# Kernel tuning notes

Measured on AMD Instinct MI355X. Metric: run time of the kernel, lower is better.

Reference implementation:

```python
import jax, jax.numpy as jnp
import numpy as np

B, S, D_MODEL, N_HEADS = 4, 2048, 512, 2
D4 = D_MODEL * 4            # output dim of quaternion projections (2048)
HD = D4 // N_HEADS          # per-head dim (1024)
EPS = 1e-6


def quat_linear(x, W, b):
    """Hamilton-product quaternion linear.
    x: [..., 4*in_q] (quaternions interleaved r,i,j,k)
    W: [4, out_q, in_q] components (r,i,j,k); b: [4*out_q]
    returns [..., 4*out_q]
    """
    xq = x.reshape(x.shape[:-1] + (-1, 4))
    xr, xi, xj, xk = xq[..., 0], xq[..., 1], xq[..., 2], xq[..., 3]
    Wr, Wi, Wj, Wk = W[0], W[1], W[2], W[3]
    m = lambda a, M: jnp.einsum('...i,oi->...o', a, M)
    o_r = m(xr, Wr) - m(xi, Wi) - m(xj, Wj) - m(xk, Wk)
    o_i = m(xr, Wi) + m(xi, Wr) + m(xj, Wk) - m(xk, Wj)
    o_j = m(xr, Wj) - m(xi, Wk) + m(xj, Wr) + m(xk, Wi)
    o_k = m(xr, Wk) + m(xi, Wj) - m(xj, Wi) + m(xk, Wr)
    out = jnp.stack([o_r, o_i, o_j, o_k], axis=-1)
    return out.reshape(out.shape[:-2] + (-1,)) + b


def setup_inputs() -> dict:
    rng = jax.random.key(0)
    ks = jax.random.split(rng, 12)
    def w(k, out_q, in_q):
        return jax.random.normal(k, (4, out_q, in_q), jnp.float32) * (1.0 / np.sqrt(4.0 * in_q))
    in_q_small = D_MODEL // 4   # q/k/v projections: d_model reals -> d_model quaternions
    in_q_big = D4 // 4          # later projections: 4*d_model reals -> d_model quaternions
    zb = jnp.zeros((D4,), jnp.float32)
    return {
        'query': jax.random.normal(ks[0], (B, S, D_MODEL), jnp.float32),
        'key':   jax.random.normal(ks[1], (B, S, D_MODEL), jnp.float32),
        'value': jax.random.normal(ks[2], (B, S, D_MODEL), jnp.float32),
        'Wq': w(ks[3], D_MODEL, in_q_small), 'bq': zb,
        'Wk': w(ks[4], D_MODEL, in_q_small), 'bk': zb,
        'Wv': w(ks[5], D_MODEL, in_q_small), 'bv': zb,
        'alpha': jax.random.normal(ks[6], (D4,), jnp.float32) * 0.1,
        'Wint': w(ks[7], D_MODEL, in_q_big), 'bint': zb,
        'Wfin': w(ks[8], D_MODEL, in_q_big), 'bfin': zb,
        'Wout': w(ks[9], D_MODEL, in_q_big), 'bout': zb,
    }


def reference(query, key, value, Wq, bq, Wk, bk, Wv, bv, alpha,
              Wint, bint, Wfin, bfin, Wout, bout):
    Q = quat_linear(query, Wq, bq).reshape(B, S, N_HEADS, HD)
    K = quat_linear(key, Wk, bk).reshape(B, S, N_HEADS, HD)
    V = quat_linear(value, Wv, bv).reshape(B, S, N_HEADS, HD)

    # spectral attention: FFT correlation + adaptive spectral filter
    Qf = jnp.fft.fft(Q, axis=1)
    Kf = jnp.fft.fft(K, axis=1)
    corr = Qf * jnp.conj(Kf)                        # [B,S,H,HD] complex64
    freqs = jnp.abs(jnp.fft.fftfreq(S))             # [S]
    phase = jnp.arctan(jnp.log(freqs + EPS))        # [S]
    a = alpha.reshape(N_HEADS, HD)
    filt = jnp.exp(1j * (phase[:, None, None] * a[None, :, :]))  # [S,H,HD]
    attn_w = jnp.fft.ifft(corr * filt[None], axis=1).real        # [B,S,H,HD]
    attn = (attn_w * V).reshape(B, S, -1)           # [B,S,4*d_model]

    attn = quat_linear(attn, Wint, bint)
    attn = quat_linear(attn, Wfin, bfin)
    return quat_linear(attn, Wout, bout)            # [B,S,4*d_model]
```

## Files before the change

kernel.cpp:

```cpp
#include <hip/hip_runtime.h>
#include <hip/hip_bf16.h>
#include <cstdint>

typedef unsigned short u16;
typedef u16  u16x4 __attribute__((ext_vector_type(4)));
typedef u16  u16x8 __attribute__((ext_vector_type(8)));
typedef short s16x8 __attribute__((ext_vector_type(8)));
typedef float f32x4 __attribute__((ext_vector_type(4)));

#define PI_F 3.14159265358979323846f
#define PD(i) ((i) + 3 * ((i) >> 5))

static __device__ __forceinline__ u16 f2bf(float f) {
    union { float f; unsigned u; } v; v.f = f;
    unsigned r = v.u + 0x7fffu + ((v.u >> 16) & 1u);
    return (u16)(r >> 16);
}
static __device__ __forceinline__ float bf2f(u16 h) {
    union { unsigned u; float f; } v; v.u = ((unsigned)h) << 16;
    return v.f;
}

__device__ __forceinline__ void gl_lds16(const u16* g, u16* l) {
    __builtin_amdgcn_global_load_lds(
        (const __attribute__((address_space(1))) unsigned int*)g,
        (__attribute__((address_space(3))) unsigned int*)l, 16, 0, 0);
}

__device__ __forceinline__ void cvt_body(int blk, const float* __restrict__ in,
                                         u16* __restrict__ o) {
    int i = blk * 256 + threadIdx.x;
    float4 a = ((const float4*)in)[2 * i];
    float4 b = ((const float4*)in)[2 * i + 1];
    u16x8 vv;
    vv[0] = f2bf(a.x); vv[1] = f2bf(a.y); vv[2] = f2bf(a.z); vv[3] = f2bf(a.w);
    vv[4] = f2bf(b.x); vv[5] = f2bf(b.y); vv[6] = f2bf(b.z); vv[7] = f2bf(b.w);
    ((u16x8*)o)[i] = vv;
}

__device__ __forceinline__ void hamilton(int c, int cp, int& qmv, float& qsv) {
    const int   qm[4][4] = {{0,1,2,3},{1,0,3,2},{2,3,0,1},{3,2,1,0}};
    const float qs[4][4] = {{1.f,-1.f,-1.f,-1.f},{1.f,1.f,1.f,-1.f},
                            {1.f,-1.f,1.f,1.f},{1.f,1.f,-1.f,1.f}};
    qmv = qm[c][cp]; qsv = qs[c][cp];
}

template<int LOGK>
__device__ __forceinline__ void e3_body(int blk, const float* __restrict__ W,
                                        u16* __restrict__ E) {
    const int K = 1 << LOGK;
    int idx = blk * 256 + threadIdx.x;
    int n = idx >> LOGK, k = idx & (K - 1);
    int o = n >> 2, c = n & 3, i = k >> 2, cp = k & 3;
    int qmv; float qsv; hamilton(c, cp, qmv, qsv);
    int in_q = K >> 2;
    float w = W[(size_t)qmv * 512 * in_q + (size_t)o * in_q + i] * qsv;
    E[idx] = f2bf(w);
}

__device__ __forceinline__ void ytr_body(int blk, const float* __restrict__ W,
                                         u16* __restrict__ YT) {
    int b = blk * 256 + threadIdx.x;
    int row = b >> 9, o = b & 511;
    int cb = row >> 9, i = row & 511;
    YT[b] = f2bf(W[((size_t)cb * 512 + o) * 512 + i]);
}

__device__ __forceinline__ void tabs_body(int blk, float2* __restrict__ gws,
                                          float* __restrict__ ph) {
    int i = blk * 256 + threadIdx.x;
    if (i < 292) {
        int off, denom;
        if (i < 4)       { off = 0;  denom = 16;   }
        else if (i < 36) { off = 4;  denom = 128;  }
        else             { off = 36; denom = 1024; }
        float a = (-PI_F) * (float)(i - off) / (float)denom;
        gws[i] = make_float2(cosf(a), sinf(a));
    }
    if (i <= 1024) {
        ph[i] = atanf(logf((float)i * (1.0f / 2048.0f) + 1e-6f));
    }
}

__global__ __launch_bounds__(256) void fat_prep(
        const float* __restrict__ query, const float* __restrict__ key,
        const float* __restrict__ value, u16* __restrict__ Acvt,
        const float* __restrict__ Wq, const float* __restrict__ Wk,
        const float* __restrict__ Wv, u16* __restrict__ Eq,
        u16* __restrict__ Ek, u16* __restrict__ Ev,
        const float* __restrict__ Wint, const float* __restrict__ Wfin,
        const float* __restrict__ Wout, u16* __restrict__ Xfin,
        u16* __restrict__ Xout, u16* __restrict__ YtInt,
        float2* __restrict__ gws, float* __restrict__ pht) {
    int b = blockIdx.x;
    if (b < 6144) {
        int ten = b >> 11, r = b & 2047;
        const float* in = (ten == 0) ? query : (ten == 1) ? key : value;
        cvt_body(r, in, Acvt + (size_t)ten * 8192 * 512);
    } else if (b < 18432) {
        int rb = b - 6144;
        int y = rb >> 12, r = rb & 4095;
        e3_body<9>(r, (y == 0) ? Wq : (y == 1) ? Wk : Wv,
                   (y == 0) ? Eq : (y == 1) ? Ek : Ev);
    } else if (b < 18944) {
        cvt_body(b - 18432, Wfin, Xfin);
    } else if (b < 19456) {
        cvt_body(b - 18944, Wout, Xout);
    } else if (b < 23552) {
        ytr_body(b - 19456, Wint, YtInt);
    } else {
        tabs_body(b - 23552, gws, pht);
    }
}

__device__ __forceinline__ void mvW_body(int blk, const float* __restrict__ v,
                                         const float* __restrict__ W,
                                         const float* __restrict__ badd,
                                         float* __restrict__ out) {
    int n    = (blk * 256 + threadIdx.x) >> 6;
    int lane = threadIdx.x & 63;
    if (n >= 2048) return;
    int o = n >> 2, c = n & 3;
    int cp = lane & 3;
    int qmv; float qsv; hamilton(c, cp, qmv, qsv);
    const float* Wrow = W + ((size_t)qmv * 512 + o) * 512;
    float s = 0.f;
    for (int k = lane; k < 2048; k += 64) s += v[k] * Wrow[k >> 2];
    s *= qsv;
#pragma unroll
    for (int off = 32; off; off >>= 1) s += __shfl_down(s, off, 64);
    if (lane == 0) out[n] = s + badd[n];
}

template<int K, int OUTMODE, int NBY>
__device__ __forceinline__ void gemm_body(int bid, u16* As, u16* Bs,
                                          const u16* __restrict__ A,
                                          const u16* __restrict__ E,
                                          const float* __restrict__ bias,
                                          void* __restrict__ outp) {
    const int t    = threadIdx.x;
    const int lane = t & 63, wave = t >> 6;
    const int wr   = wave >> 1, wc = wave & 1;
    const int lr   = lane & 15, kg = lane >> 4;
    const int l7   = lr & 7;

    constexpr int SPX = (4 * (NBY / 4)) / 8;
    const int xcd = bid & 7, p = bid >> 3;
    const int st  = xcd * SPX + (p >> 4);
    const int w   = p & 15;
    const int bx  = (st & 3) * 4 + (w & 3);
    const int by  = (st >> 2) * 4 + (w >> 2);
    const int m0  = by * 128;
    const int n0  = bx * 128;

    f32x4 acc[4][4];
#pragma unroll
    for (int i = 0; i < 4; ++i)
#pragma unroll
        for (int j = 0; j < 4; ++j) acc[i][j] = (f32x4){0.f, 0.f, 0.f, 0.f};

    const int arow = wr * 64 + lr;
    const int brow = wc * 64 + lr;

    for (int k0 = 0; k0 < K; k0 += 64) {
#pragma unroll
        for (int c = 0; c < 4; ++c) {
            int idx = t + c * 256;
            int row = idx >> 3, sl = idx & 7;
            int gsl = sl ^ (row & 7);
            gl_lds16(A + (size_t)(m0 + row) * K + k0 + gsl * 8, &As[idx * 8]);
            gl_lds16(E + (size_t)(n0 + row) * K + k0 + gsl * 8, &Bs[idx * 8]);
        }
        __syncthreads();
#pragma unroll
        for (int ks = 0; ks < 2; ++ks) {
            const int slot = (ks * 4 + kg) ^ l7;
            s16x8 av[4], bv[4];
#pragma unroll
            for (int mi = 0; mi < 4; ++mi)
                av[mi] = *(const s16x8*)&As[(arow + mi * 16) * 64 + slot * 8];
#pragma unroll
            for (int ni = 0; ni < 4; ++ni)
                bv[ni] = *(const s16x8*)&Bs[(brow + ni * 16) * 64 + slot * 8];
#pragma unroll
            for (int mi = 0; mi < 4; ++mi)
#pragma unroll
                for (int ni = 0; ni < 4; ++ni)
                    acc[mi][ni] = __builtin_amdgcn_mfma_f32_16x16x32_bf16(
                        av[mi], bv[ni], acc[mi][ni], 0, 0, 0);
        }
        __syncthreads();
    }

#pragma unroll
    for (int ni = 0; ni < 4; ++ni) {
        int n = n0 + wc * 64 + ni * 16 + lr;
        float bvl = bias ? bias[n] : 0.0f;
#pragma unroll
        for (int mi = 0; mi < 4; ++mi) {
#pragma unroll
            for (int r = 0; r < 4; ++r) {
                int m = m0 + wr * 64 + mi * 16 + kg * 4 + r;
                float val = acc[mi][ni][r] + bvl;
                if constexpr (OUTMODE == 0) {
                    ((u16*)outp)[(size_t)m * 2048 + n] = f2bf(val);
                } else if constexpr (OUTMODE == 1) {
                    ((float*)outp)[(size_t)m * 2048 + n] = val;
                } else {
                    int b = m >> 11, s = m & 2047;
                    ((u16*)outp)[((size_t)b * 2048 + n) * 2048 + s] = f2bf(val);
                }
            }
        }
    }
}

template<int K, int OUTMODE, int NBY>
__global__ __launch_bounds__(256) void gemm2(const u16* __restrict__ A,
                                             const u16* __restrict__ E,
                                             const float* __restrict__ bias,
                                             void* __restrict__ outp) {
    __shared__ u16 As[128 * 64];
    __shared__ u16 Bs[128 * 64];
    gemm_body<K, OUTMODE, NBY>(blockIdx.x, As, Bs, A, E, bias, outp);
}

__global__ __launch_bounds__(256) void gemm_fatA(const u16* __restrict__ Aq,
                                                 const u16* __restrict__ Eq,
                                                 const float* __restrict__ bq,
                                                 void* __restrict__ Qt,
                                                 const u16* __restrict__ Ak,
                                                 const u16* __restrict__ Ek,
                                                 const float* __restrict__ bk,
                                                 void* __restrict__ Kt,
                                                 const u16* __restrict__ Xfin,
                                                 const u16* __restrict__ YtInt,
                                                 void* __restrict__ Z1,
                                                 const float* __restrict__ Wfin,
                                                 const float* __restrict__ bint,
                                                 const float* __restrict__ bfin,
                                                 float* __restrict__ bv1) {
    __shared__ u16 As[128 * 64];
    __shared__ u16 Bs[128 * 64];
    int bid = blockIdx.x;
    if (bid < 256) {
        gemm_body<512, 0, 16>(bid, As, Bs, Xfin, YtInt, nullptr, Z1);
    } else if (bid < 1280) {
        gemm_body<512, 2, 64>(bid - 256, As, Bs, Aq, Eq, bq, Qt);
    } else if (bid < 2304) {
        gemm_body<512, 2, 64>(bid - 1280, As, Bs, Ak, Ek, bk, Kt);
    } else {
        mvW_body(bid - 2304, bint, Wfin, bfin, bv1);
    }
}

__global__ __launch_bounds__(256) void qcomb1(const u16* __restrict__ Z1,
                                              u16* __restrict__ Yt2) {
    __shared__ float tile[32][33];
    const int CA[4][4] = {{0,1,2,3},{1,0,3,2},{2,0,1,3},{3,0,2,1}};
    const int CB[4][4] = {{0,1,2,3},{0,1,2,3},{0,2,3,1},{0,3,1,2}};
    const float SG[4][4] = {{1.f,-1.f,-1.f,-1.f},{1.f,1.f,1.f,-1.f},
                            {1.f,1.f,1.f,-1.f},{1.f,1.f,1.f,-1.f}};
    const int cm = blockIdx.z;
    const int p0 = blockIdx.x * 32, i0 = blockIdx.y * 32;
    const int tx = threadIdx.x, ty = threadIdx.y;
#pragma unroll
    for (int dy = 0; dy < 32; dy += 8) {
        int p = p0 + ty + dy;
        float acc = 0.f;
#pragma unroll
        for (int q = 0; q < 4; ++q)
            acc += SG[cm][q] * bf2f(Z1[(size_t)(CA[cm][q] * 512 + p) * 2048
                                       + CB[cm][q] * 512 + i0 + tx]);
        tile[ty + dy][tx] = acc;
    }
    __syncthreads();
#pragma unroll
    for (int dy = 0; dy < 32; dy += 8)
        Yt2[((size_t)cm * 512 + i0 + ty + dy) * 512 + p0 + tx]
            = f2bf(tile[tx][ty + dy]);
}

template<int LH, int OFF>
__device__ __forceinline__ void r8pass(float* re, float* im,
                                       const float2* __restrict__ wt, int t) {
    constexpr int h = 1 << LH;
    __syncthreads();
    const int j  = t & (h - 1);
    const int i0 = ((t >> LH) << (LH + 3)) | j;
    const float2 w = wt[OFF + j];
    const float t2r = w.x * w.x - w.y * w.y;
    const float t2i = 2.f * w.x * w.y;
    const float t1r = t2r * t2r - t2i * t2i;
    const float t1i = 2.f * t2r * t2i;
    const float S = 0.70710678118654752f;
    const float Ac = S * (w.x + w.y);
    const float Bc = S * (w.y - w.x);

    float xr[8], xi[8];
    int p[8];
#pragma unroll
    for (int k = 0; k < 8; ++k) {
        p[k] = PD(i0 + k * h);
        xr[k] = re[p[k]]; xi[k] = im[p[k]];
    }
#pragma unroll
    for (int kp = 0; kp < 8; kp += 2) {
        float tr = t1r * xr[kp + 1] - t1i * xi[kp + 1];
        float ti = t1r * xi[kp + 1] + t1i * xr[kp + 1];
        float ar = xr[kp], ai = xi[kp];
        xr[kp] = ar + tr;     xi[kp] = ai + ti;
        xr[kp + 1] = ar - tr; xi[kp + 1] = ai - ti;
    }
#pragma unroll
    for (int q = 0; q < 2; ++q) {
        int b0 = q * 4;
        {
            float tr = t2r * xr[b0 + 2] - t2i * xi[b0 + 2];
            float ti = t2r * xi[b0 + 2] + t2i * xr[b0 + 2];
            float ar = xr[b0], ai = xi[b0];
            xr[b0] = ar + tr;     xi[b0] = ai + ti;
            xr[b0 + 2] = ar - tr; xi[b0 + 2] = ai - ti;
        }
        {
            float tr = t2i * xr[b0 + 3] + t2r * xi[b0 + 3];
            float ti = t2i * xi[b0 + 3] - t2r * xr[b0 + 3];
            float ar = xr[b0 + 1], ai = xi[b0 + 1];
            xr[b0 + 1] = ar + tr; xi[b0 + 1] = ai + ti;
            xr[b0 + 3] = ar - tr; xi[b0 + 3] = ai - ti;
        }
    }
    {
        float tr = w.x * xr[4] - w.y * xi[4];
        float ti = w.x * xi[4] + w.y * xr[4];
        float ar = xr[0], ai = xi[0];
        xr[0] = ar + tr; xi[0] = ai + ti;
        xr[4] = ar - tr; xi[4] = ai - ti;
    }
    {
        float tr = Ac * xr[5] - Bc * xi[5];
        float ti = Ac * xi[5] + Bc * xr[5];
        float ar = xr[1], ai = xi[1];
        xr[1] = ar + tr; xi[1] = ai + ti;
        xr[5] = ar - tr; xi[5] = ai - ti;
    }
    {
        float tr = w.y * xr[6] + w.x * xi[6];
        float ti = w.y * xi[6] - w.x * xr[6];
        float ar = xr[2], ai = xi[2];
        xr[2] = ar + tr; xi[2] = ai + ti;
        xr[6] = ar - tr; xi[6] = ai - ti;
    }
    {
        float tr = Bc * xr[7] + Ac * xi[7];
        float ti = Bc * xi[7] - Ac * xr[7];
        float ar = xr[3], ai = xi[3];
        xr[3] = ar + tr; xi[3] = ai + ti;
        xr[7] = ar - tr; xi[7] = ai - ti;
    }
#pragma unroll
    for (int k = 0; k < 8; ++k) { re[p[k]] = xr[k]; im[p[k]] = xi[k]; }
}

__device__ void fft2048(float* re, float* im, const float2* __restrict__ wt, int t) {
    __syncthreads();
#pragma unroll
    for (int u = 0; u < 2; ++u) {
        int i0 = (t + u * 256) << 2;
        int p0 = PD(i0);
        float x0r = re[p0],     x0i = im[p0];
        float x1r = re[p0 + 1], x1i = im[p0 + 1];
        float x2r = re[p0 + 2], x2i = im[p0 + 2];
        float x3r = re[p0 + 3], x3i = im[p0 + 3];
        float ar = x0r + x1r, ai = x0i + x1i;
        float br = x0r - x1r, bi = x0i - x1i;
        float cr = x2r + x3r, ci = x2i + x3i;
        float dr = x2r - x3r, di = x2i - x3i;
        re[p0]     = ar + cr; im[p0]     = ai + ci;
        re[p0 + 2] = ar - cr; im[p0 + 2] = ai - ci;
        re[p0 + 1] = br + di; im[p0 + 1] = bi - dr;
        re[p0 + 3] = br - di; im[p0 + 3] = bi + dr;
    }
    r8pass<2, 0>(re, im, wt, t);
    r8pass<5, 4>(re, im, wt, t);
    r8pass<8, 36>(re, im, wt, t);
    __syncthreads();
}

__device__ void spectral_body(int sbid, float* zre, float* zim, float2* wt,
                              const u16* __restrict__ Qt,
                              const u16* __restrict__ Kt,
                              u16* __restrict__ Wt,
                              const float* __restrict__ alpha,
                              const float2* __restrict__ gws,
                              const float* __restrict__ gph) {
    const int t  = threadIdx.x;
    const int b  = sbid >> 10;
    const int cp = sbid & 1023;
    const int c0 = cp * 2;
    const size_t base0 = ((size_t)b * 2048 + c0) * 2048;
    const size_t base1 = base0 + 2048;

    for (int i = t; i < 292; i += 256) wt[i] = gws[i];

    float ph[4];
    float PH1r[4], PH1i[4], PH2r[4], PH2i[4];
    float ph24 = 0.f, PH24_1 = 0.f, PH24_2 = 0.f;

#pragma unroll
    for (int ch = 0; ch < 2; ++ch) {
        const size_t base = ch ? base1 : base0;
        const u16* Qp = Qt + base;
        const u16* Kp = Kt + base;
        __syncthreads();
#pragma unroll
        for (int u = 0; u < 8; ++u) {
            int s = t + u * 256;
            int r = __brev((unsigned)s) >> 21;
            zre[PD(r)] = bf2f(Qp[s]);
            zim[PD(r)] = bf2f(Kp[s]);
        }
        fft2048(zre, zim, wt, t);
        const float ac = alpha[c0 + ch];
#pragma unroll
        for (int u = 0; u < 4; ++u) {
            int k = t + u * 256;
            int m = (2048 - k) & 2047;
            float ar = zre[PD(k)], ai = zim[PD(k)];
            float br = zre[PD(m)], bi = zim[PD(m)];
            float qr = 0.5f * (ar + br), qi = 0.5f * (ai - bi);
            float kr = 0.5f * (ai + bi), ki = 0.5f * (br - ar);
            float cr = qr * kr + qi * ki;
            float ci = qi * kr - qr * ki;
            if (ch == 0) ph[u] = gph[min(k, 2048 - k)];
            float fr, fi;
            __sincosf(ph[u] * ac, &fi, &fr);
            float Pkr = cr * fr - ci * fi, Pki = cr * fi + ci * fr;
            float qr2 = 0.5f * (br + ar), qi2 = 0.5f * (bi - ai);
            float kr2 = 0.5f * (bi + ai), ki2 = 0.5f * (ar - br);
            float cr2 = qr2 * kr2 + qi2 * ki2;
            float ci2 = qi2 * kr2 - qr2 * ki2;
            float Pmr = cr2 * fr - ci2 * fi, Pmi = cr2 * fi + ci2 * fr;
            float hr = 0.5f * (Pkr + Pmr), hi = 0.5f * (Pki - Pmi);
            if (ch == 0) { PH1r[u] = hr; PH1i[u] = hi; }
            else         { PH2r[u] = hr; PH2i[u] = hi; }
        }
        if (t == 0) {
            float ar = zre[PD(1024)], ai = zim[PD(1024)];
            float cr = ar * ai;
            if (ch == 0) ph24 = gph[1024];
            float fr, fi;
            __sincosf(ph24 * ac, &fi, &fr);
            if (ch == 0) PH24_1 = cr * fr; else PH24_2 = cr * fr;
        }
    }

    __syncthreads();
#pragma unroll
    for (int u = 0; u < 4; ++u) {
        int k = t + u * 256;
        int m = (2048 - k) & 2047;
        int rk = __brev((unsigned)k) >> 21;
        int rm = __brev((unsigned)m) >> 21;
        zre[PD(rk)] = PH1r[u] - PH2i[u];
        zim[PD(rk)] = PH1i[u] + PH2r[u];
        zre[PD(rm)] = PH1r[u] + PH2i[u];
        zim[PD(rm)] = PH2r[u] - PH1i[u];
    }
    if (t == 0) {
        zre[PD(1)] = PH24_1;
        zim[PD(1)] = PH24_2;
    }
    fft2048(zre, zim, wt, t);

#pragma unroll
    for (int u = 0; u < 8; ++u) {
        int s = t + u * 256;
        int j = (2048 - s) & 2047;
        Wt[base0 + s] = f2bf(zre[PD(j)] * (1.0f / 2048.0f));
        Wt[base1 + s] = f2bf(zim[PD(j)] * (1.0f / 2048.0f));
    }
}

__global__ __launch_bounds__(256) void fat_specv(const u16* __restrict__ Qt,
                                                 const u16* __restrict__ Kt,
                                                 u16* __restrict__ Wt,
                                                 const float* __restrict__ alpha,
                                                 const float2* __restrict__ gws,
                                                 const float* __restrict__ gph,
                                                 const u16* __restrict__ Av,
                                                 const u16* __restrict__ Ev,
                                                 const float* __restrict__ bvb,
                                                 void* __restrict__ Vt,
                                                 const u16* __restrict__ Xout,
                                                 const u16* __restrict__ Yt2,
                                                 void* __restrict__ Z2,
                                                 const float* __restrict__ Wout,
                                                 const float* __restrict__ bv1,
                                                 const float* __restrict__ bout,
                                                 float* __restrict__ bv2) {
    __shared__ __align__(16) char smem[32768];
    int bid = blockIdx.x;
    if (bid < 256) {
        gemm_body<512, 0, 16>(bid, (u16*)smem, (u16*)(smem + 16384),
                              Xout, Yt2, nullptr, Z2);
        return;
    }
    if (bid >= 5376) {
        mvW_body(bid - 5376, bv1, Wout, bout, bv2);
        return;
    }
    bid -= 256;
    if (bid % 5 == 4) {
        gemm_body<512, 2, 64>(bid / 5, (u16*)smem, (u16*)(smem + 16384),
                              Av, Ev, bvb, Vt);
    } else {
        int sbid = (bid / 5) * 4 + (bid % 5);
        spectral_body(sbid, (float*)smem, (float*)(smem + 8960),
                      (float2*)(smem + 17920), Qt, Kt, Wt, alpha, gws, gph);
    }
}

__device__ __forceinline__ void qcomb2_body(int blk, const u16* __restrict__ Z2,
                                            u16* __restrict__ Ecomb) {
    int id = blk * 256 + threadIdx.x;
    int q = id >> 9, i = id & 511;
    float z[4][4];
#pragma unroll
    for (int ca = 0; ca < 4; ++ca)
#pragma unroll
        for (int cb = 0; cb < 4; ++cb)
            z[ca][cb] = bf2f(Z2[(size_t)(ca * 512 + q) * 2048 + cb * 512 + i]);
    float wc[4];
    wc[0] = z[0][0] - z[1][1] - z[2][2] - z[3][3];
    wc[1] = z[1][0] + z[0][1] + z[3][2] - z[2][3];
    wc[2] = z[2][0] + z[0][2] + z[1][3] - z[3][1];
    wc[3] = z[3][0] + z[0][3] + z[2][1] - z[1][2];
#pragma unroll
    for (int c = 0; c < 4; ++c) {
        u16x4 row;
#pragma unroll
        for (int cp = 0; cp < 4; ++cp) {
            int qmv; float qsv; hamilton(c, cp, qmv, qsv);
            row[cp] = f2bf(qsv * wc[qmv]);
        }
        *(u16x4*)&Ecomb[(size_t)(4 * q + c) * 2048 + 4 * i] = row;
    }
}

__device__ __forceinline__ void tmul_body(int blk, const u16* __restrict__ W,
                                          const u16* __restrict__ V,
                                          u16* __restrict__ out, u16* tile) {
    const int b  = blk >> 10;
    const int rem = blk & 1023;
    const int c0 = (rem & 31) * 64, s0 = (rem >> 5) * 64;
    const int t  = threadIdx.x;
    const int g  = (t & 15) * 4;
    const int rb = t >> 4;
#pragma unroll
    for (int r = 0; r < 4; ++r) {
        int c = rb + 16 * r;
        size_t idx = ((size_t)b * 2048 + c0 + c) * 2048 + s0 + g;
        u16x4 wv = *(const u16x4*)&W[idx];
        u16x4 vv = *(const u16x4*)&V[idx];
#pragma unroll
        for (int j = 0; j < 4; ++j)
            tile[c * 70 + g + j] = f2bf(bf2f(wv[j]) * bf2f(vv[j]));
    }
    __syncthreads();
#pragma unroll
    for (int r = 0; r < 4; ++r) {
        int s = rb + 16 * r;
        u16x4 o;
#pragma unroll
        for (int j = 0; j < 4; ++j) o[j] = tile[(g + j) * 70 + s];
        *(u16x4*)&out[((size_t)b * 2048 + s0 + s) * 2048 + c0 + g] = o;
    }
}

__global__ __launch_bounds__(256) void fat_post(const u16* __restrict__ Z2,
                                                u16* __restrict__ Ecomb,
                                                const u16* __restrict__ W,
                                                const u16* __restrict__ V,
                                                u16* __restrict__ attn) {
    __shared__ u16 tile[64 * 70];
    int bid = blockIdx.x;
    if (bid < 1024) qcomb2_body(bid, Z2, Ecomb);
    else            tmul_body(bid - 1024, W, V, attn, tile);
}

extern "C" void kernel_launch(void* const* d_in, const int* in_sizes, int n_in,
                              void* d_out, int out_size, void* d_ws, size_t ws_size,
                              hipStream_t stream) {
    const float* query = (const float*)d_in[0];
    const float* key   = (const float*)d_in[1];
    const float* value = (const float*)d_in[2];
    const float* Wq    = (const float*)d_in[3];
    const float* bq    = (const float*)d_in[4];
    const float* Wk    = (const float*)d_in[5];
    const float* bk    = (const float*)d_in[6];
    const float* Wv    = (const float*)d_in[7];
    const float* bv    = (const float*)d_in[8];
    const float* alpha = (const float*)d_in[9];
    const float* Wint  = (const float*)d_in[10];
    const float* bint  = (const float*)d_in[11];
    const float* Wfin  = (const float*)d_in[12];
    const float* bfin  = (const float*)d_in[13];
    const float* Wout  = (const float*)d_in[14];
    const float* bout  = (const float*)d_in[15];

    char* ws = (char*)d_ws;
    size_t off = 0;
    auto alloc = [&](size_t bytes) -> void* {
        void* p = ws + off;
        off += (bytes + 255) & ~(size_t)255;
        return p;
    };
    u16* Eq    = (u16*)alloc((size_t)2048 * 512 * 2);
    u16* Ek    = (u16*)alloc((size_t)2048 * 512 * 2);
    u16* Ev    = (u16*)alloc((size_t)2048 * 512 * 2);
    u16* Xfin  = (u16*)alloc((size_t)2048 * 512 * 2);
    u16* Xout  = (u16*)alloc((size_t)2048 * 512 * 2);
    u16* YtInt = (u16*)alloc((size_t)2048 * 512 * 2);
    u16* Yt2   = (u16*)alloc((size_t)2048 * 512 * 2);
    u16* Z1    = (u16*)alloc((size_t)2048 * 2048 * 2);
    u16* Z2    = (u16*)alloc((size_t)2048 * 2048 * 2);
    u16* Ecomb = (u16*)alloc((size_t)2048 * 2048 * 2);
    u16* Qt    = (u16*)alloc((size_t)4 * 2048 * 2048 * 2);
    u16* Kt    = (u16*)alloc((size_t)4 * 2048 * 2048 * 2);
    u16* Vt    = (u16*)alloc((size_t)4 * 2048 * 2048 * 2);
    u16* attn  = (u16*)alloc((size_t)8192 * 2048 * 2);
    float2* gws = (float2*)alloc(292 * 8);
    float*  pht = (float*)alloc(1025 * 4);
    float*  bv1 = (float*)alloc(2048 * 4);
    float*  bv2 = (float*)alloc(2048 * 4);
    u16* Wt = Qt;
    u16* Aq = attn;
    u16* Ak = attn + (size_t)8192 * 512;
    u16* Av = attn + (size_t)8192 * 1024;

    fat_prep<<<23557, 256, 0, stream>>>(query, key, value, Aq,
                                        Wq, Wk, Wv, Eq, Ek, Ev,
                                        Wint, Wfin, Wout, Xfin, Xout, YtInt,
                                        gws, pht);

    gemm_fatA<<<2816, 256, 0, stream>>>(Aq, Eq, bq, Qt, Ak, Ek, bk, Kt,
                                        Xfin, YtInt, Z1, Wfin, bint, bfin, bv1);

    qcomb1<<<dim3(16, 16, 4), dim3(32, 8), 0, stream>>>(Z1, Yt2);

    fat_specv<<<5888, 256, 0, stream>>>(Qt, Kt, Wt, alpha, gws, pht,
                                        Av, Ev, bv, Vt, Xout, Yt2, Z2,
                                        Wout, bv1, bout, bv2);

    fat_post<<<5120, 256, 0, stream>>>(Z2, Ecomb, Wt, Vt, attn);

    gemm2<2048, 1, 64><<<1024, 256, 0, stream>>>(attn, Ecomb, bv2, (float*)d_out);
}
```

Baseline: 306.7 us.

## Use 64x64 GEMM tiles in fused spectral/V-projection kernel to cut LDS footprint

Adds a 64x64-tile GEMM body with a 2x2 MFMA per wave and uses it for the Z2 and V-projection GEMMs inside the fused spectral kernel. The block layout changes so spectral and V-GEMM blocks interleave 1:1 instead of 4:1, and the shared memory buffer shrinks from 32 KB to 20 KB. The aim is higher occupancy and better load balance across the heterogeneous blocks. The cost is less data reuse per tile and more blocks re-reading operands.

Result: slower. 321.1 us, median of 2 (+4.7%).

```diff
diff --git a/kernel.cpp b/kernel.cpp
--- a/kernel.cpp
+++ b/kernel.cpp
@@ -215,6 +215,90 @@
     }
 }
 
+template<int K, int OUTMODE, int NBX, int NBY>
+__device__ __forceinline__ void gemm64_body(int bid, u16* As, u16* Bs,
+                                            const u16* __restrict__ A,
+                                            const u16* __restrict__ E,
+                                            const float* __restrict__ bias,
+                                            void* __restrict__ outp) {
+    const int t    = threadIdx.x;
+    const int lane = t & 63, wave = t >> 6;
+    const int wr   = wave >> 1, wc = wave & 1;
+    const int lr   = lane & 15, kg = lane >> 4;
+    const int l7   = lr & 7;
+
+    constexpr int STC = NBX / 4;
+    constexpr int SPX = (STC * (NBY / 4)) / 8;
+    const int xcd = bid & 7, p = bid >> 3;
+    const int st  = xcd * SPX + (p >> 4);
+    const int w   = p & 15;
+    const int bx  = (st % STC) * 4 + (w & 3);
+    const int by  = (st / STC) * 4 + (w >> 2);
+    const int m0  = by * 64;
+    const int n0  = bx * 64;
+
+    f32x4 acc[2][2];
+#pragma unroll
+    for (int i = 0; i < 2; ++i)
+#pragma unroll
+        for (int j = 0; j < 2; ++j) acc[i][j] = (f32x4){0.f, 0.f, 0.f, 0.f};
+
+    const int arow = wr * 32 + lr;
+    const int brow = wc * 32 + lr;
+
+    for (int k0 = 0; k0 < K; k0 += 64) {
+#pragma unroll
+        for (int c = 0; c < 2; ++c) {
+            int idx = t + c * 256;
+            int row = idx >> 3, sl = idx & 7;
+            int gsl = sl ^ (row & 7);
+            gl_lds16(A + (size_t)(m0 + row) * K + k0 + gsl * 8, &As[idx * 8]);
+            gl_lds16(E + (size_t)(n0 + row) * K + k0 + gsl * 8, &Bs[idx * 8]);
+        }
+        __syncthreads();
+#pragma unroll
+        for (int ks = 0; ks < 2; ++ks) {
+            const int slot = (ks * 4 + kg) ^ l7;
+            s16x8 av[2], bv[2];
+#pragma unroll
+            for (int mi = 0; mi < 2; ++mi)
+                av[mi] = *(const s16x8*)&As[(arow + mi * 16) * 64 + slot * 8];
+#pragma unroll
+            for (int ni = 0; ni < 2; ++ni)
+                bv[ni] = *(const s16x8*)&Bs[(brow + ni * 16) * 64 + slot * 8];
+#pragma unroll
+            for (int mi = 0; mi < 2; ++mi)
+#pragma unroll
+                for (int ni = 0; ni < 2; ++ni)
+                    acc[mi][ni] = __builtin_amdgcn_mfma_f32_16x16x32_bf16(
+                        av[mi], bv[ni], acc[mi][ni], 0, 0, 0);
+        }
+        __syncthreads();
+    }
+
+#pragma unroll
+    for (int ni = 0; ni < 2; ++ni) {
+        int n = n0 + wc * 32 + ni * 16 + lr;
+        float bvl = bias ? bias[n] : 0.0f;
+#pragma unroll
+        for (int mi = 0; mi < 2; ++mi) {
+#pragma unroll
+            for (int r = 0; r < 4; ++r) {
+                int m = m0 + wr * 32 + mi * 16 + kg * 4 + r;
+                float val = acc[mi][ni][r] + bvl;
+                if constexpr (OUTMODE == 0) {
+                    ((u16*)outp)[(size_t)m * 2048 + n] = f2bf(val);
+                } else if constexpr (OUTMODE == 1) {
+                    ((float*)outp)[(size_t)m * 2048 + n] = val;
+                } else {
+                    int b = m >> 11, s = m & 2047;
+                    ((u16*)outp)[((size_t)b * 2048 + n) * 2048 + s] = f2bf(val);
+                }
+            }
+        }
+    }
+}
+
 template<int K, int OUTMODE, int NBY>
 __global__ __launch_bounds__(256) void gemm2(const u16* __restrict__ A,
                                              const u16* __restrict__ E,
@@ -499,24 +583,23 @@
                                                  const float* __restrict__ bv1,
                                                  const float* __restrict__ bout,
                                                  float* __restrict__ bv2) {
-    __shared__ __align__(16) char smem[32768];
+    __shared__ __align__(16) char smem[20480];
     int bid = blockIdx.x;
-    if (bid < 256) {
-        gemm_body<512, 0, 16>(bid, (u16*)smem, (u16*)(smem + 16384),
-                              Xout, Yt2, nullptr, Z2);
+    if (bid < 1024) {
+        gemm64_body<512, 0, 32, 32>(bid, (u16*)smem, (u16*)(smem + 8192),
+                                    Xout, Yt2, nullptr, Z2);
         return;
     }
-    if (bid >= 5376) {
-        mvW_body(bid - 5376, bv1, Wout, bout, bv2);
+    if (bid >= 9216) {
+        mvW_body(bid - 9216, bv1, Wout, bout, bv2);
         return;
     }
-    bid -= 256;
-    if (bid % 5 == 4) {
-        gemm_body<512, 2, 64>(bid / 5, (u16*)smem, (u16*)(smem + 16384),
-                              Av, Ev, bvb, Vt);
+    bid -= 1024;
+    if (bid & 1) {
+        gemm64_body<512, 2, 32, 128>(bid >> 1, (u16*)smem, (u16*)(smem + 8192),
+                                     Av, Ev, bvb, Vt);
     } else {
-        int sbid = (bid / 5) * 4 + (bid % 5);
-        spectral_body(sbid, (float*)smem, (float*)(smem + 8960),
+        spectral_body(bid >> 1, (float*)smem, (float*)(smem + 8960),
                       (float2*)(smem + 17920), Qt, Kt, Wt, alpha, gws, gph);
     }
 }
@@ -649,7 +732,7 @@
 
     qcomb1<<<dim3(16, 16, 4), dim3(32, 8), 0, stream>>>(Z1, Yt2);
 
-    fat_specv<<<5888, 256, 0, stream>>>(Qt, Kt, Wt, alpha, gws, pht,
+    fat_specv<<<9728, 256, 0, stream>>>(Qt, Kt, Wt, alpha, gws, pht,
                                         Av, Ev, bv, Vt, Xout, Yt2, Z2,
                                         Wout, bv1, bout, bv2);
 
```
